# Kernel optimization log

Measured on AMD Instinct MI355X. Metric: run time of the kernel, lower is better.

The kernel has to match this reference:

```python
import jax, jax.numpy as jnp
import numpy as np

N, E, DIN, GB, GD, LB, LD, G = 50000, 640000, 64, 128, 4, 256, 2, 1024


def setup_inputs() -> dict:
    key = jax.random.key(0)
    ks = jax.random.split(key, 20)
    p = lambda k, shape: (jax.random.normal(k, shape, dtype=jnp.float32) * 0.05)
    return {
        "x": jax.random.normal(ks[0], (N, DIN), dtype=jnp.float32),
        "edge_index": jax.random.randint(ks[1], (2, E), 0, N, dtype=jnp.int64),
        "batch": jnp.sort(jax.random.randint(ks[2], (N,), 0, G, dtype=jnp.int64)),
        "num_graphs": G,
        "W0": p(ks[3], (DIN, GB)), "b0": p(ks[4], (GB,)),
        "Wg": p(ks[5], (GD, GB, GB)), "bg": p(ks[6], (GD, GB)),
        "gamma_g": jnp.ones((GD, GB), jnp.float32), "beta_g": jnp.zeros((GD, GB), jnp.float32),
        "Wl0": p(ks[7], (GB, LB)), "bl0": p(ks[8], (LB,)),
        "Wl": p(ks[9], (LD, LB, LB)), "bl": p(ks[10], (LD, LB)),
        "gamma_l": jnp.ones((LD, LB), jnp.float32), "beta_l": jnp.zeros((LD, LB), jnp.float32),
        "Wout": p(ks[11], (LB, 2)), "bout": p(ks[12], (2,)),
    }


def reference(x, edge_index, batch, num_graphs, W0, b0, Wg, bg, gamma_g, beta_g,
              Wl0, bl0, Wl, bl, gamma_l, beta_l, Wout, bout):
    n = x.shape[0]
    src, dst = edge_index[0], edge_index[1]
    # GCN degree normalization with self loops: deg = 1 + in-degree
    deg = jax.ops.segment_sum(jnp.ones(src.shape[0], x.dtype), dst, num_segments=n) + 1.0
    dinv = jax.lax.rsqrt(deg)                 # deg^{-1/2}
    enorm = dinv[src] * dinv[dst]             # [E] edge norm
    snorm = dinv * dinv                       # [N] self-loop norm (deg^{-1})

    def gcn(h, W, b):
        hw = h @ W                                            # [N, GB]
        agg = jax.ops.segment_sum(hw[src] * enorm[:, None], dst, num_segments=n)
        return agg + hw * snorm[:, None] + b

    def bn(h, g, bt):  # training-mode batchnorm (biased var), eps=1e-5
        m = h.mean(0)
        v = h.var(0)
        return (h - m) * jax.lax.rsqrt(v + 1e-5) * g + bt

    h = jax.nn.relu(gcn(x, W0, b0))
    for i in range(Wg.shape[0]):
        h = jax.nn.relu(bn(gcn(h, Wg[i], bg[i]), gamma_g[i], beta_g[i]))
    # global_add_pool
    hp = jax.ops.segment_sum(h, batch, num_segments=num_graphs)  # [G, GB]
    h = jax.nn.relu(hp @ Wl0 + bl0)
    for i in range(Wl.shape[0]):
        h = jax.nn.relu(bn(h @ Wl[i] + bl[i], gamma_l[i], beta_l[i]))
    return h @ Wout + bout
```

## Files before the change

### kernel.cpp

```cpp
#include <hip/hip_runtime.h>

#define NN 50000
#define EE 640000
#define DINv 64
#define GBv 128
#define GDv 4
#define LBv 256
#define LDv 2
#define GGv 1024

#define NB 196
#define BCAP 4096
#define BTILE 4096
#define NBT ((EE + BTILE - 1) / BTILE)

#define NTILES ((NN + 63) / 64)
#define UPN (NN * 16)
#define CONVN (DINv * GBv + GDv * GBv * GBv)

typedef _Float16 f16x8 __attribute__((ext_vector_type(8)));
typedef float f32x4 __attribute__((ext_vector_type(4)));

__device__ __forceinline__ float h2f(ushort u) {
  union { ushort u; _Float16 h; } x;
  x.u = u;
  return (float)x.h;
}
__device__ __forceinline__ ushort f2h(float f) {
  union { ushort u; _Float16 h; } x;
  x.h = (_Float16)f;
  return x.u;
}


__global__ __launch_bounds__(256) void k_bucket(const int* __restrict__ ei,
                                                int* __restrict__ bcnt,
                                                uint* __restrict__ bkt) {
  __shared__ int lcnt[NB];
  __shared__ int lbase[NB];
  __shared__ int gbase[NB];
  __shared__ int ls[256];
  __shared__ uint stage[BTILE];
  __shared__ ushort sb[BTILE];
  int tid = threadIdx.x;
  int t0 = blockIdx.x * BTILE;
  int cnt = min(BTILE, EE - t0);
  for (int i = tid; i < NB; i += 256) lcnt[i] = 0;
  __syncthreads();

  uint en[16];
  int bb[16], rk[16];
  int nper = (cnt + 255) >> 8;
  for (int k = 0; k < nper; k++) {
    int e = k * 256 + tid;
    if (e < cnt) {
      int src = ei[t0 + e];
      int dst = ei[EE + t0 + e];
      int b = dst >> 8;
      en[k] = ((uint)src << 8) | (uint)(dst & 255);
      bb[k] = b;
      rk[k] = atomicAdd(&lcnt[b], 1);
    } else {
      bb[k] = -1;
    }
  }
  __syncthreads();

  int v = (tid < NB) ? lcnt[tid] : 0;
  ls[tid] = v;
  __syncthreads();
  for (int off = 1; off < 256; off <<= 1) {
    int t = (tid >= off) ? ls[tid - off] : 0;
    __syncthreads();
    ls[tid] += t;
    __syncthreads();
  }
  if (tid < NB) {
    lbase[tid] = ls[tid] - v;
    gbase[tid] = atomicAdd(&bcnt[tid], v);
  }
  __syncthreads();

  for (int k = 0; k < nper; k++) {
    if (bb[k] >= 0) {
      int slot = lbase[bb[k]] + rk[k];
      stage[slot] = en[k];
      sb[slot] = (ushort)bb[k];
    }
  }
  __syncthreads();

  for (int i = tid; i < cnt; i += 256) {
    int b = sb[i];
    bkt[(size_t)b * BCAP + gbase[b] + (i - lbase[b])] = stage[i];
  }
}

__global__ __launch_bounds__(256) void k_bscan(const int* __restrict__ bcnt,
                                               int* __restrict__ bbase,
                                               int* __restrict__ offs) {
  __shared__ int ls[256];
  int tid = threadIdx.x;
  int v = (tid < NB) ? bcnt[tid] : 0;
  ls[tid] = v;
  __syncthreads();
  for (int off = 1; off < 256; off <<= 1) {
    int t = (tid >= off) ? ls[tid - off] : 0;
    __syncthreads();
    ls[tid] += t;
    __syncthreads();
  }
  if (tid < NB) bbase[tid] = ls[tid] - v;
  if (tid == 0) offs[NN] = EE;
}


__global__ __launch_bounds__(256) void k_csr(const uint* __restrict__ bkt,
                                             const int* __restrict__ bcnt,
                                             const int* __restrict__ bbase,
                                             int* __restrict__ offs,
                                             float* __restrict__ dinv,
                                             int* __restrict__ col,
                                             int* __restrict__ deg,
                                             int* __restrict__ ghist) {
  __shared__ int lhist[256];
  __shared__ int lofs[256];
  __shared__ int lcur[256];
  __shared__ int lh2[64];
  int b = blockIdx.x;
  int cnt = bcnt[b], base = bbase[b];
  const uint* B = bkt + (size_t)b * BCAP;
  int tid = threadIdx.x;
  lhist[tid] = 0;
  if (tid < 64) lh2[tid] = 0;
  __syncthreads();
  for (int i = tid; i < cnt; i += 256) atomicAdd(&lhist[B[i] & 255], 1);
  __syncthreads();
  int v = lhist[tid];
  lofs[tid] = v;
  __syncthreads();
  for (int off = 1; off < 256; off <<= 1) {
    int t = (tid >= off) ? lofs[tid - off] : 0;
    __syncthreads();
    lofs[tid] += t;
    __syncthreads();
  }
  int excl = lofs[tid] - v;
  int n = b * 256 + tid;
  if (n < NN) {
    offs[n] = base + excl;
    dinv[n] = rsqrtf((float)(v + 1));
    int d = min(v, 63);
    deg[n] = d;
    atomicAdd(&lh2[d], 1);
  }
  lcur[tid] = excl;
  __syncthreads();
  if (tid < 64 && lh2[tid]) atomicAdd(&ghist[tid], lh2[tid]);
  for (int i = tid; i < cnt; i += 256) {
    uint e = B[i];
    int p = atomicAdd(&lcur[e & 255], 1);
    col[base + p] = (int)(e >> 8);
  }
}

__global__ void k_dscan(const int* __restrict__ ghist, int* __restrict__ dcur) {
  if (threadIdx.x == 0 && blockIdx.x == 0) {
    int run = 0;
    for (int i = 0; i < 64; i++) {
      dcur[i] = run;
      run += ghist[i];
    }
  }
}

__global__ __launch_bounds__(256) void k_dperm(const int* __restrict__ deg,
                                               int* __restrict__ dcur,
                                               int* __restrict__ perm) {
  __shared__ int lhist[64];
  __shared__ int lbase[64];
  int tid = threadIdx.x;
  if (tid < 64) lhist[tid] = 0;
  __syncthreads();
  int n = blockIdx.x * 256 + tid;
  int d = 0, rk = 0;
  if (n < NN) {
    d = deg[n];
    rk = atomicAdd(&lhist[d], 1);
  }
  __syncthreads();
  if (tid < 64 && lhist[tid]) lbase[tid] = atomicAdd(&dcur[tid], lhist[tid]);
  __syncthreads();
  if (n < NN) perm[lbase[d] + rk] = n;
}


__global__ __launch_bounds__(256) void k_prep(const float* __restrict__ x,
                                              const float* __restrict__ dinv,
                                              const float* __restrict__ W0,
                                              const float* __restrict__ Wg,
                                              ushort* __restrict__ u,
                                              ushort* __restrict__ Wt0,
                                              ushort* __restrict__ Wtg) {
  int idx = blockIdx.x * 256 + threadIdx.x;
  if (idx < UPN) {
    int n = idx >> 4;
    float4 v = ((const float4*)x)[idx];
    float d = dinv[n];
    union { ushort us[4]; uint2 q; } o;
    o.us[0] = f2h(v.x * d);
    o.us[1] = f2h(v.y * d);
    o.us[2] = f2h(v.z * d);
    o.us[3] = f2h(v.w * d);
    ((uint2*)u)[idx] = o.q;
  } else {
    int j = idx - UPN;
    if (j < DINv * GBv) {
      int c = j >> 6, k = j & 63;
      Wt0[j] = f2h(W0[k * GBv + c]);
    } else if (j < CONVN) {
      int e = j - DINv * GBv;
      int i = e >> 14, rem = e & 16383;
      int c = rem >> 7, k = rem & 127;
      Wtg[e] = f2h(Wg[i * GBv * GBv + k * GBv + c]);
    }
  }
}


template <int K, int MODE>
__global__ __launch_bounds__(256) void k_agg(const ushort* __restrict__ Gin,
                                             const int* __restrict__ col,
                                             const int* __restrict__ offs,
                                             const float* __restrict__ dinv,
                                             const int* __restrict__ perm,
                                             const float* __restrict__ st,
                                             const float* __restrict__ gamma,
                                             const float* __restrict__ beta,
                                             ushort* __restrict__ V) {
  constexpr int VEC = K / 16;
  __shared__ float sS[128], sT[128];
  int tid = threadIdx.x;
  if constexpr (MODE == 2) {
    if (tid < 128) {
      float mu = st[tid] * (1.f / NN);
      float var = st[128 + tid] * (1.f / NN) - mu * mu;
      float s = rsqrtf(var + 1e-5f) * gamma[tid];
      sS[tid] = s;
      sT[tid] = beta[tid] - mu * s;
    }
    __syncthreads();
  }
  int lane = tid & 63;
  int q = lane >> 4, m = lane & 15;
  int idx = blockIdx.x * 16 + (tid >> 6) * 4 + q;
  int n = perm[idx];

  float sc[VEC], tc[VEC];
  if constexpr (MODE == 2) {
#pragma unroll
    for (int v = 0; v < VEC; v++) {
      sc[v] = sS[m * VEC + v];
      tc[v] = sT[m * VEC + v];
    }
  }

  union U { uint4 v4; uint2 v2; ushort us[8]; };
  auto loadrow = [&](int s) {
    U u;
    const ushort* p = Gin + (long)s * K + m * VEC;
    if constexpr (VEC == 8) u.v4 = *(const uint4*)p;
    else u.v2 = *(const uint2*)p;
    return u;
  };
  float acc[VEC];
#pragma unroll
  for (int v = 0; v < VEC; v++) acc[v] = 0.f;
  auto addrow = [&](U u, float dv) {
#pragma unroll
    for (int v = 0; v < VEC; v++) {
      float g = h2f(u.us[v]);
      if constexpr (MODE == 0) acc[v] += g;
      else if constexpr (MODE == 1) acc[v] += fmaxf(g, 0.f) * dv;
      else acc[v] += fmaxf(g * sc[v] + tc[v], 0.f) * dv;
    }
  };

  float dn = dinv[n];
  addrow(loadrow(n), dn);

  int s0 = offs[n], s1 = offs[n + 1];
  int j = s0;
  for (; j + 7 < s1; j += 8) {
    int si[8];
#pragma unroll
    for (int t = 0; t < 8; t++) si[t] = col[j + t];
    U uu[8];
#pragma unroll
    for (int t = 0; t < 8; t++) uu[t] = loadrow(si[t]);
    float dd[8];
#pragma unroll
    for (int t = 0; t < 8; t++) dd[t] = (MODE != 0) ? dinv[si[t]] : 0.f;
#pragma unroll
    for (int t = 0; t < 8; t++) addrow(uu[t], dd[t]);
  }
  for (; j + 3 < s1; j += 4) {
    int si[4];
#pragma unroll
    for (int t = 0; t < 4; t++) si[t] = col[j + t];
    U uu[4];
#pragma unroll
    for (int t = 0; t < 4; t++) uu[t] = loadrow(si[t]);
    float dd[4];
#pragma unroll
    for (int t = 0; t < 4; t++) dd[t] = (MODE != 0) ? dinv[si[t]] : 0.f;
#pragma unroll
    for (int t = 0; t < 4; t++) addrow(uu[t], dd[t]);
  }
  for (; j < s1; j++) {
    int s = col[j];
    U u = loadrow(s);
    float dv = (MODE != 0) ? dinv[s] : 0.f;
    addrow(u, dv);
  }

  U o;
#pragma unroll
  for (int v = 0; v < VEC; v++) o.us[v] = f2h(acc[v] * dn);
  ushort* op = V + (long)n * K + m * VEC;
  if constexpr (VEC == 8) *(uint4*)op = o.v4;
  else *(uint2*)op = o.v2;
}


template <int K, bool STATS>
__global__ __launch_bounds__(256) void k_mm(const ushort* __restrict__ X,
                                            const ushort* __restrict__ Wt,
                                            const float* __restrict__ bias,
                                            float* __restrict__ stG,
                                            ushort* __restrict__ Gout) {
  constexpr int KP = K + 8;
  constexpr int CP = 136;
  constexpr bool REUSE = (K == 128);
  __shared__ __attribute__((aligned(16))) _Float16 sW[128 * KP];
  __shared__ __attribute__((aligned(16))) _Float16 sA[64 * KP];
  __shared__ __attribute__((aligned(16))) _Float16 sCbuf[REUSE ? 8 : 64 * CP];
  __shared__ float sB[128];
  __shared__ float ssum[128], ssq[128];
  _Float16* sC = REUSE ? sA : sCbuf;
  int tid = threadIdx.x;

  {
    constexpr int CH = K / 8;
    for (int i = tid; i < 128 * CH; i += 256) {
      int c = i / CH, ch = i - c * CH;
      *(uint4*)&sW[c * KP + ch * 8] = ((const uint4*)Wt)[i];
    }
  }
  if (tid < 128) {
    sB[tid] = bias[tid];
    if constexpr (STATS) {
      ssum[tid] = 0.f;
      ssq[tid] = 0.f;
    }
  }

  int w = tid >> 6, lane = tid & 63;
  int m = lane & 15, quad = lane >> 4;
  int crow = 16 * w + quad * 4;

  float ps[8], pq[8];
  if constexpr (STATS) {
#pragma unroll
    for (int ct = 0; ct < 8; ct++) { ps[ct] = 0.f; pq[ct] = 0.f; }
  }

  for (int tile = blockIdx.x; tile < NTILES; tile += gridDim.x) {
    int row0 = tile * 64;
    __syncthreads();

    {
      int r = tid >> 2, col0 = (tid & 3) * (K / 4);
      int gr = row0 + r;
      const uint4* p = (const uint4*)(X + (long)gr * K + col0);
#pragma unroll
      for (int ch = 0; ch < K / 32; ch++) {
        uint4 v = (gr < NN) ? p[ch] : make_uint4(0, 0, 0, 0);
        *(uint4*)&sA[r * KP + col0 + ch * 8] = v;
      }
    }
    __syncthreads();

    f32x4 acc[8];
#pragma unroll
    for (int ct = 0; ct < 8; ct++) acc[ct] = (f32x4){0.f, 0.f, 0.f, 0.f};
    const _Float16* pa = &sA[(16 * w + m) * KP + quad * 8];
#pragma unroll
    for (int ks = 0; ks < K; ks += 32) {
      f16x8 a = *(const f16x8*)(pa + ks);
#pragma unroll
      for (int ct = 0; ct < 8; ct++) {
        f16x8 b = *(const f16x8*)&sW[(ct * 16 + m) * KP + ks + quad * 8];
        acc[ct] = __builtin_amdgcn_mfma_f32_16x16x32_f16(a, b, acc[ct], 0, 0, 0);
      }
    }

    if constexpr (STATS) {
#pragma unroll
      for (int ct = 0; ct < 8; ct++) {
        int c = ct * 16 + m;
        float b = sB[c];
#pragma unroll
        for (int r = 0; r < 4; r++) {
          if (row0 + crow + r < NN) {
            float g = acc[ct][r] + b;
            ps[ct] += g;
            pq[ct] += g * g;
          }
        }
      }
    }
    if constexpr (REUSE) __syncthreads();

#pragma unroll
    for (int ct = 0; ct < 8; ct++) {
      int c = ct * 16 + m;
      float b = sB[c];
#pragma unroll
      for (int r = 0; r < 4; r++) sC[(crow + r) * CP + c] = (_Float16)(acc[ct][r] + b);
    }
    __syncthreads();

    {
      int r = tid >> 2, col0 = (tid & 3) * 32;
      int gr = row0 + r;
      if (gr < NN) {
        const uint4* src = (const uint4*)&sC[r * CP + col0];
        uint4* dst = (uint4*)(Gout + (long)gr * 128 + col0);
#pragma unroll
        for (int ch = 0; ch < 4; ch++) dst[ch] = src[ch];
      }
    }
  }

  if constexpr (STATS) {
#pragma unroll
    for (int ct = 0; ct < 8; ct++) {
      float s = ps[ct], q = pq[ct];
      s += __shfl_xor(s, 16);
      q += __shfl_xor(q, 16);
      s += __shfl_xor(s, 32);
      q += __shfl_xor(q, 32);
      if (quad == 0) {
        atomicAdd(&ssum[ct * 16 + m], s);
        atomicAdd(&ssq[ct * 16 + m], q);
      }
    }
    __syncthreads();
    if (tid < 128) {
      int c = (tid + blockIdx.x * 8) & 127;
      atomicAdd(&stG[c], ssum[c]);
      atomicAdd(&stG[128 + c], ssq[c]);
    }
  }
}


__global__ __launch_bounds__(128) void k_pool2(const ushort* __restrict__ G,
                                               const float* __restrict__ st,
                                               const float* __restrict__ gamma,
                                               const float* __restrict__ beta,
                                               const int* __restrict__ batch,
                                               float* __restrict__ hp) {
  __shared__ int sse[2];
  int g = blockIdx.x;
  int c = threadIdx.x;
  if (c < 2) {
    int key = g + c;
    int lo = 0, hi = NN;
    while (lo < hi) {
      int mid = (lo + hi) >> 1;
      if (batch[mid] < key) lo = mid + 1;
      else hi = mid;
    }
    sse[c] = lo;
  }
  __syncthreads();
  int s = sse[0], e = sse[1];
  float m = st[c] * (1.f / NN);
  float v = st[128 + c] * (1.f / NN) - m * m;
  float sc = rsqrtf(v + 1e-5f) * gamma[c];
  float tc = beta[c] - m * sc;
  float acc = 0.f;
  for (int n = s; n < e; n++) acc += fmaxf(h2f(G[(long)n * 128 + c]) * sc + tc, 0.f);
  hp[(long)g * 128 + c] = acc;
}


__global__ void k_colstats(const float* __restrict__ X, int rows, float* __restrict__ st) {
  int c = threadIdx.x;
  int C = blockDim.x;
  float s = 0.f, q = 0.f;
  for (int r = blockIdx.x; r < rows; r += gridDim.x) {
    float v = X[(long)r * C + c];
    s += v;
    q += v * v;
  }
  atomicAdd(&st[c], s);
  atomicAdd(&st[C + c], q);
}


template <int KIN, int MODE>
__global__ __launch_bounds__(256) void k_fc(const float* __restrict__ X,
                                            const float* __restrict__ W,
                                            const float* __restrict__ b,
                                            const float* __restrict__ st,
                                            const float* __restrict__ gamma,
                                            const float* __restrict__ beta,
                                            float* __restrict__ Y) {
  __shared__ float sx[KIN];
  int g = blockIdx.x;
  int c = threadIdx.x;
  for (int k = c; k < KIN; k += 256) {
    float v = X[(long)g * KIN + k];
    if constexpr (MODE == 2) {
      float m = st[k] * (1.f / GGv);
      float var = st[KIN + k] * (1.f / GGv) - m * m;
      v = fmaxf((v - m) * rsqrtf(var + 1e-5f) * gamma[k] + beta[k], 0.f);
    }
    sx[k] = v;
  }
  __syncthreads();
  float acc = b[c];
#pragma unroll 8
  for (int k = 0; k < KIN; k++) acc += sx[k] * W[(long)k * 256 + c];
  Y[(long)g * 256 + c] = (MODE == 0) ? fmaxf(acc, 0.f) : acc;
}

__global__ __launch_bounds__(256) void k_out(const float* __restrict__ X,
                                             const float* __restrict__ st,
                                             const float* __restrict__ gamma,
                                             const float* __restrict__ beta,
                                             const float* __restrict__ Wout,
                                             const float* __restrict__ bout,
                                             float* __restrict__ out) {
  int g = blockIdx.x * 4 + (threadIdx.x >> 6);
  int l = threadIdx.x & 63;
  float a0 = 0.f, a1 = 0.f;
  for (int k = l; k < LBv; k += 64) {
    float z = X[(long)g * LBv + k];
    float m = st[k] * (1.f / GGv);
    float var = st[LBv + k] * (1.f / GGv) - m * m;
    float x = fmaxf((z - m) * rsqrtf(var + 1e-5f) * gamma[k] + beta[k], 0.f);
    a0 += x * Wout[2 * k];
    a1 += x * Wout[2 * k + 1];
  }
  for (int off = 32; off > 0; off >>= 1) {
    a0 += __shfl_down(a0, off);
    a1 += __shfl_down(a1, off);
  }
  if (l == 0) {
    out[2 * g] = a0 + bout[0];
    out[2 * g + 1] = a1 + bout[1];
  }
}


extern "C" void kernel_launch(void* const* d_in, const int* in_sizes, int n_in,
                              void* d_out, int out_size, void* d_ws, size_t ws_size,
                              hipStream_t stream) {
  const float* x = (const float*)d_in[0];
  const int* ei = (const int*)d_in[1];
  const int* batch = (const int*)d_in[2];
  const float* W0 = (const float*)d_in[4];
  const float* b0 = (const float*)d_in[5];
  const float* Wg = (const float*)d_in[6];
  const float* bg = (const float*)d_in[7];
  const float* gamma_g = (const float*)d_in[8];
  const float* beta_g = (const float*)d_in[9];
  const float* Wl0 = (const float*)d_in[10];
  const float* bl0 = (const float*)d_in[11];
  const float* Wl = (const float*)d_in[12];
  const float* bl = (const float*)d_in[13];
  const float* gamma_l = (const float*)d_in[14];
  const float* beta_l = (const float*)d_in[15];
  const float* Wout = (const float*)d_in[16];
  const float* bout = (const float*)d_in[17];
  float* out = (float*)d_out;

  char* w = (char*)d_ws;
  auto alloc = [&](size_t bytes) {
    void* p = (void*)w;
    w += (bytes + 255) & ~(size_t)255;
    return p;
  };
  int* bcnt = (int*)alloc((size_t)NB * 4);
  float* stAll = (float*)alloc((size_t)(4 * 256 + 2 * 512) * 4);
  int* ghist = (int*)alloc((size_t)64 * 4);
  size_t zspan = (char*)w - (char*)bcnt;
  uint* bkt = (uint*)alloc((size_t)NB * BCAP * 4);
  int* bbase = (int*)alloc((size_t)NB * 4);
  int* offs = (int*)alloc((size_t)(NN + 1) * 4);
  int* col = (int*)alloc((size_t)EE * 4);
  float* dinv = (float*)alloc((size_t)NN * 4);
  int* deg = (int*)alloc((size_t)NN * 4);
  int* perm = (int*)alloc((size_t)NN * 4);
  int* dcur = (int*)alloc((size_t)64 * 4);
  ushort* u = (ushort*)alloc((size_t)NN * DINv * 2);
  ushort* V = (ushort*)alloc((size_t)NN * GBv * 2);
  ushort* g = (ushort*)alloc((size_t)NN * GBv * 2);
  ushort* Wt0 = (ushort*)alloc((size_t)DINv * GBv * 2);
  ushort* Wtg = (ushort*)alloc((size_t)GDv * GBv * GBv * 2);
  float* hp = (float*)alloc((size_t)GGv * GBv * 4);
  float* m1 = (float*)alloc((size_t)GGv * LBv * 4);
  float* m2 = (float*)alloc((size_t)GGv * LBv * 4);

  float* stg = stAll;
  float* sth0 = stAll + 4 * 256;
  float* sth1 = sth0 + 512;

  hipMemsetAsync(bcnt, 0, zspan, stream);

  k_bucket<<<NBT, 256, 0, stream>>>(ei, bcnt, bkt);
  k_bscan<<<1, 256, 0, stream>>>(bcnt, bbase, offs);
  k_csr<<<NB, 256, 0, stream>>>(bkt, bcnt, bbase, offs, dinv, col, deg, ghist);
  k_dscan<<<1, 64, 0, stream>>>(ghist, dcur);
  k_dperm<<<NB, 256, 0, stream>>>(deg, dcur, perm);
  k_prep<<<(UPN + CONVN + 255) / 256, 256, 0, stream>>>(x, dinv, W0, Wg, u, Wt0, Wtg);

  const int AGG = NN / 16;
  const int MMG = 512;

  k_agg<64, 0><<<AGG, 256, 0, stream>>>(u, col, offs, dinv, perm, nullptr, nullptr,
                                        nullptr, V);
  k_mm<64, false><<<MMG, 256, 0, stream>>>(V, Wt0, b0, nullptr, g);

  k_agg<128, 1><<<AGG, 256, 0, stream>>>(g, col, offs, dinv, perm, nullptr, nullptr,
                                         nullptr, V);
  k_mm<128, true><<<MMG, 256, 0, stream>>>(V, Wtg, bg, stg, g);

  for (int i = 1; i < GDv; i++) {
    k_agg<128, 2><<<AGG, 256, 0, stream>>>(g, col, offs, dinv, perm,
                                           stg + (size_t)(i - 1) * 256,
                                           gamma_g + (size_t)(i - 1) * GBv,
                                           beta_g + (size_t)(i - 1) * GBv, V);
    k_mm<128, true><<<MMG, 256, 0, stream>>>(V, Wtg + (size_t)i * GBv * GBv,
                                             bg + (size_t)i * GBv, stg + (size_t)i * 256, g);
  }

  k_pool2<<<GGv, 128, 0, stream>>>(g, stg + 3 * 256, gamma_g + 3 * GBv, beta_g + 3 * GBv,
                                   batch, hp);

  k_fc<GBv, 0><<<GGv, 256, 0, stream>>>(hp, Wl0, bl0, nullptr, nullptr, nullptr, m1);
  k_fc<LBv, 1><<<GGv, 256, 0, stream>>>(m1, Wl, bl, nullptr, nullptr, nullptr, m2);
  k_colstats<<<256, LBv, 0, stream>>>(m2, GGv, sth0);
  k_fc<LBv, 2><<<GGv, 256, 0, stream>>>(m2, Wl + (size_t)LBv * LBv, bl + LBv, sth0,
                                        gamma_l, beta_l, m1);
  k_colstats<<<256, LBv, 0, stream>>>(m1, GGv, sth1);
  k_out<<<GGv / 4, 256, 0, stream>>>(m1, sth1, gamma_l + LBv, beta_l + LBv, Wout, bout, out);
}
```

Baseline: 449.0 us.

## Fuse neighbor aggregation with MFMA matmul per layer and fold scan kernels

Each GCN layer's sparse aggregation now writes its 64-row tile straight into shared memory, and the same block then runs the MFMA matmul and writes the output rows scattered via perm. This removes the intermediate V round-trip through global memory and one launch per layer. The bucket scan and degree scan kernels are also folded into k_csr and k_dperm, which each recompute a small prefix sum redundantly per block. The cost is that every block reloads the weight matrix into LDS, and the per-block LDS footprint may reduce occupancy for the latency-bound gather phase. Output buffers now ping-pong between g1 and g2.

```diff
diff --git a/kernel.cpp b/kernel.cpp
--- a/kernel.cpp
+++ b/kernel.cpp
@@ -96,28 +96,9 @@
   }
 }
 
-__global__ __launch_bounds__(256) void k_bscan(const int* __restrict__ bcnt,
-                                               int* __restrict__ bbase,
-                                               int* __restrict__ offs) {
-  __shared__ int ls[256];
-  int tid = threadIdx.x;
-  int v = (tid < NB) ? bcnt[tid] : 0;
-  ls[tid] = v;
-  __syncthreads();
-  for (int off = 1; off < 256; off <<= 1) {
-    int t = (tid >= off) ? ls[tid - off] : 0;
-    __syncthreads();
-    ls[tid] += t;
-    __syncthreads();
-  }
-  if (tid < NB) bbase[tid] = ls[tid] - v;
-  if (tid == 0) offs[NN] = EE;
-}
-
 
 __global__ __launch_bounds__(256) void k_csr(const uint* __restrict__ bkt,
                                              const int* __restrict__ bcnt,
-                                             const int* __restrict__ bbase,
                                              int* __restrict__ offs,
                                              float* __restrict__ dinv,
                                              int* __restrict__ col,
@@ -126,14 +107,24 @@
   __shared__ int lhist[256];
   __shared__ int lofs[256];
   __shared__ int lcur[256];
+  __shared__ int lsb[256];
   __shared__ int lh2[64];
   int b = blockIdx.x;
-  int cnt = bcnt[b], base = bbase[b];
-  const uint* B = bkt + (size_t)b * BCAP;
   int tid = threadIdx.x;
+  int bv = (tid < NB) ? bcnt[tid] : 0;
+  lsb[tid] = bv;
   lhist[tid] = 0;
   if (tid < 64) lh2[tid] = 0;
   __syncthreads();
+  for (int off = 1; off < 256; off <<= 1) {
+    int t = (tid >= off) ? lsb[tid - off] : 0;
+    __syncthreads();
+    lsb[tid] += t;
+    __syncthreads();
+  }
+  int cnt = bcnt[b];
+  int base = lsb[b] - cnt;
+  const uint* B = bkt + (size_t)b * BCAP;
   for (int i = tid; i < cnt; i += 256) atomicAdd(&lhist[B[i] & 255], 1);
   __syncthreads();
   int v = lhist[tid];
@@ -157,6 +148,7 @@
   lcur[tid] = excl;
   __syncthreads();
   if (tid < 64 && lh2[tid]) atomicAdd(&ghist[tid], lh2[tid]);
+  if (b == 0 && tid == 0) offs[NN] = EE;
   for (int i = tid; i < cnt; i += 256) {
     uint e = B[i];
     int p = atomicAdd(&lcur[e & 255], 1);
@@ -164,18 +156,10 @@
   }
 }
 
-__global__ void k_dscan(const int* __restrict__ ghist, int* __restrict__ dcur) {
-  if (threadIdx.x == 0 && blockIdx.x == 0) {
-    int run = 0;
-    for (int i = 0; i < 64; i++) {
-      dcur[i] = run;
-      run += ghist[i];
-    }
-  }
-}
 
 __global__ __launch_bounds__(256) void k_dperm(const int* __restrict__ deg,
-                                               int* __restrict__ dcur,
+                                               const int* __restrict__ ghist,
+                                               int* __restrict__ gcur,
                                                int* __restrict__ perm) {
   __shared__ int lhist[64];
   __shared__ int lbase[64];
@@ -189,7 +173,11 @@
     rk = atomicAdd(&lhist[d], 1);
   }
   __syncthreads();
-  if (tid < 64 && lhist[tid]) lbase[tid] = atomicAdd(&dcur[tid], lhist[tid]);
+  if (tid < 64) {
+    int s = 0;
+    for (int i = tid + 1; i < 64; i++) s += ghist[i];
+    if (lhist[tid]) lbase[tid] = s + atomicAdd(&gcur[tid], lhist[tid]);
+  }
   __syncthreads();
   if (n < NN) perm[lbase[d] + rk] = n;
 }
@@ -228,33 +216,57 @@
 }
 
 
-template <int K, int MODE>
-__global__ __launch_bounds__(256) void k_agg(const ushort* __restrict__ Gin,
-                                             const int* __restrict__ col,
-                                             const int* __restrict__ offs,
-                                             const float* __restrict__ dinv,
-                                             const int* __restrict__ perm,
-                                             const float* __restrict__ st,
-                                             const float* __restrict__ gamma,
-                                             const float* __restrict__ beta,
-                                             ushort* __restrict__ V) {
+template <int K, int MODE, bool STATS>
+__global__ __launch_bounds__(256) void k_layer(const ushort* __restrict__ Gin,
+                                               const int* __restrict__ col,
+                                               const int* __restrict__ offs,
+                                               const float* __restrict__ dinv,
+                                               const int* __restrict__ perm,
+                                               const float* __restrict__ st,
+                                               const float* __restrict__ gamma,
+                                               const float* __restrict__ beta,
+                                               const ushort* __restrict__ Wt,
+                                               const float* __restrict__ bias,
+                                               float* __restrict__ stG,
+                                               ushort* __restrict__ Gout) {
   constexpr int VEC = K / 16;
-  __shared__ float sS[128], sT[128];
+  constexpr int KP = K + 8;
+  constexpr int CP = 136;
+  constexpr bool REUSE = (K == 128);
+  __shared__ __attribute__((aligned(16))) _Float16 sW[128 * KP];
+  __shared__ __attribute__((aligned(16))) _Float16 sA[64 * KP];
+  __shared__ __attribute__((aligned(16))) _Float16 sCbuf[REUSE ? 8 : 64 * CP];
+  __shared__ float sB[128], sS[128], sT[128];
+  __shared__ float ssum[128], ssq[128];
+  _Float16* sC = REUSE ? sA : sCbuf;
   int tid = threadIdx.x;
-  if constexpr (MODE == 2) {
-    if (tid < 128) {
+
+  {
+    constexpr int CH = K / 8;
+    for (int i = tid; i < 128 * CH; i += 256) {
+      int c = i / CH, ch = i - c * CH;
+      *(uint4*)&sW[c * KP + ch * 8] = ((const uint4*)Wt)[i];
+    }
+  }
+  if (tid < 128) {
+    sB[tid] = bias[tid];
+    if constexpr (STATS) {
+      ssum[tid] = 0.f;
+      ssq[tid] = 0.f;
+    }
+    if constexpr (MODE == 2) {
       float mu = st[tid] * (1.f / NN);
       float var = st[128 + tid] * (1.f / NN) - mu * mu;
       float s = rsqrtf(var + 1e-5f) * gamma[tid];
       sS[tid] = s;
       sT[tid] = beta[tid] - mu * s;
     }
-    __syncthreads();
-  }
-  int lane = tid & 63;
-  int q = lane >> 4, m = lane & 15;
-  int idx = blockIdx.x * 16 + (tid >> 6) * 4 + q;
-  int n = perm[idx];
+  }
+  if constexpr (MODE == 2) __syncthreads();
+
+  int w = tid >> 6, lane = tid & 63;
+  int quad = lane >> 4, m = lane & 15;
+  int row0 = blockIdx.x * 64;
 
   float sc[VEC], tc[VEC];
   if constexpr (MODE == 2) {
@@ -273,173 +285,124 @@
     else u.v2 = *(const uint2*)p;
     return u;
   };
-  float acc[VEC];
-#pragma unroll
-  for (int v = 0; v < VEC; v++) acc[v] = 0.f;
-  auto addrow = [&](U u, float dv) {
-#pragma unroll
-    for (int v = 0; v < VEC; v++) {
-      float g = h2f(u.us[v]);
-      if constexpr (MODE == 0) acc[v] += g;
-      else if constexpr (MODE == 1) acc[v] += fmaxf(g, 0.f) * dv;
-      else acc[v] += fmaxf(g * sc[v] + tc[v], 0.f) * dv;
-    }
-  };
-
-  float dn = dinv[n];
-  addrow(loadrow(n), dn);
-
-  int s0 = offs[n], s1 = offs[n + 1];
-  int j = s0;
-  for (; j + 7 < s1; j += 8) {
-    int si[8];
-#pragma unroll
-    for (int t = 0; t < 8; t++) si[t] = col[j + t];
-    U uu[8];
-#pragma unroll
-    for (int t = 0; t < 8; t++) uu[t] = loadrow(si[t]);
-    float dd[8];
-#pragma unroll
-    for (int t = 0; t < 8; t++) dd[t] = (MODE != 0) ? dinv[si[t]] : 0.f;
-#pragma unroll
-    for (int t = 0; t < 8; t++) addrow(uu[t], dd[t]);
-  }
-  for (; j + 3 < s1; j += 4) {
-    int si[4];
-#pragma unroll
-    for (int t = 0; t < 4; t++) si[t] = col[j + t];
-    U uu[4];
-#pragma unroll
-    for (int t = 0; t < 4; t++) uu[t] = loadrow(si[t]);
-    float dd[4];
-#pragma unroll
-    for (int t = 0; t < 4; t++) dd[t] = (MODE != 0) ? dinv[si[t]] : 0.f;
-#pragma unroll
-    for (int t = 0; t < 4; t++) addrow(uu[t], dd[t]);
-  }
-  for (; j < s1; j++) {
-    int s = col[j];
-    U u = loadrow(s);
-    float dv = (MODE != 0) ? dinv[s] : 0.f;
-    addrow(u, dv);
-  }
-
-  U o;
-#pragma unroll
-  for (int v = 0; v < VEC; v++) o.us[v] = f2h(acc[v] * dn);
-  ushort* op = V + (long)n * K + m * VEC;
-  if constexpr (VEC == 8) *(uint4*)op = o.v4;
-  else *(uint2*)op = o.v2;
-}
-
-
-template <int K, bool STATS>
-__global__ __launch_bounds__(256) void k_mm(const ushort* __restrict__ X,
-                                            const ushort* __restrict__ Wt,
-                                            const float* __restrict__ bias,
-                                            float* __restrict__ stG,
-                                            ushort* __restrict__ Gout) {
-  constexpr int KP = K + 8;
-  constexpr int CP = 136;
-  constexpr bool REUSE = (K == 128);
-  __shared__ __attribute__((aligned(16))) _Float16 sW[128 * KP];
-  __shared__ __attribute__((aligned(16))) _Float16 sA[64 * KP];
-  __shared__ __attribute__((aligned(16))) _Float16 sCbuf[REUSE ? 8 : 64 * CP];
-  __shared__ float sB[128];
-  __shared__ float ssum[128], ssq[128];
-  _Float16* sC = REUSE ? sA : sCbuf;
-  int tid = threadIdx.x;
-
-  {
-    constexpr int CH = K / 8;
-    for (int i = tid; i < 128 * CH; i += 256) {
-      int c = i / CH, ch = i - c * CH;
-      *(uint4*)&sW[c * KP + ch * 8] = ((const uint4*)Wt)[i];
-    }
-  }
-  if (tid < 128) {
-    sB[tid] = bias[tid];
-    if constexpr (STATS) {
-      ssum[tid] = 0.f;
-      ssq[tid] = 0.f;
-    }
-  }
-
-  int w = tid >> 6, lane = tid & 63;
-  int m = lane & 15, quad = lane >> 4;
+
+  for (int rnd = 0; rnd < 4; rnd++) {
+    int r = rnd * 16 + w * 4 + quad;
+    int idx = row0 + r;
+    float acc[VEC];
+#pragma unroll
+    for (int v = 0; v < VEC; v++) acc[v] = 0.f;
+    float dn = 0.f;
+    if (idx < NN) {
+      int n = perm[idx];
+      dn = dinv[n];
+      auto addrow = [&](U u, float dv) {
+#pragma unroll
+        for (int v = 0; v < VEC; v++) {
+          float g = h2f(u.us[v]);
+          if constexpr (MODE == 0) acc[v] += g;
+          else if constexpr (MODE == 1) acc[v] += fmaxf(g, 0.f) * dv;
+          else acc[v] += fmaxf(g * sc[v] + tc[v], 0.f) * dv;
+        }
+      };
+      addrow(loadrow(n), dn);
+      int s0 = offs[n], s1 = offs[n + 1];
+      int j = s0;
+      for (; j + 7 < s1; j += 8) {
+        int si[8];
+#pragma unroll
+        for (int t = 0; t < 8; t++) si[t] = col[j + t];
+        U uu[8];
+#pragma unroll
+        for (int t = 0; t < 8; t++) uu[t] = loadrow(si[t]);
+        float dd[8];
+#pragma unroll
+        for (int t = 0; t < 8; t++) dd[t] = (MODE != 0) ? dinv[si[t]] : 0.f;
+#pragma unroll
+        for (int t = 0; t < 8; t++) addrow(uu[t], dd[t]);
+      }
+      for (; j + 3 < s1; j += 4) {
+        int si[4];
+#pragma unroll
+        for (int t = 0; t < 4; t++) si[t] = col[j + t];
+        U uu[4];
+#pragma unroll
+        for (int t = 0; t < 4; t++) uu[t] = loadrow(si[t]);
+        float dd[4];
+#pragma unroll
+        for (int t = 0; t < 4; t++) dd[t] = (MODE != 0) ? dinv[si[t]] : 0.f;
+#pragma unroll
+        for (int t = 0; t < 4; t++) addrow(uu[t], dd[t]);
+      }
+      for (; j < s1; j++) {
+        int s = col[j];
+        U u = loadrow(s);
+        float dv = (MODE != 0) ? dinv[s] : 0.f;
+        addrow(u, dv);
+      }
+    }
+    U o;
+#pragma unroll
+    for (int v = 0; v < VEC; v++) o.us[v] = f2h(acc[v] * dn);
+    _Float16* ap = &sA[r * KP + m * VEC];
+    if constexpr (VEC == 8) *(uint4*)ap = o.v4;
+    else *(uint2*)ap = o.v2;
+  }
+  __syncthreads();
+
+  f32x4 acc2[8];
+#pragma unroll
+  for (int ct = 0; ct < 8; ct++) acc2[ct] = (f32x4){0.f, 0.f, 0.f, 0.f};
+  const _Float16* pa = &sA[(16 * w + m) * KP + quad * 8];
+#pragma unroll
+  for (int ks = 0; ks < K; ks += 32) {
+    f16x8 a = *(const f16x8*)(pa + ks);
+#pragma unroll
+    for (int ct = 0; ct < 8; ct++) {
+      f16x8 bfr = *(const f16x8*)&sW[(ct * 16 + m) * KP + ks + quad * 8];
+      acc2[ct] = __builtin_amdgcn_mfma_f32_16x16x32_f16(a, bfr, acc2[ct], 0, 0, 0);
+    }
+  }
+
   int crow = 16 * w + quad * 4;
-
   float ps[8], pq[8];
   if constexpr (STATS) {
 #pragma unroll
-    for (int ct = 0; ct < 8; ct++) { ps[ct] = 0.f; pq[ct] = 0.f; }
-  }
-
-  for (int tile = blockIdx.x; tile < NTILES; tile += gridDim.x) {
-    int row0 = tile * 64;
-    __syncthreads();
-
-    {
-      int r = tid >> 2, col0 = (tid & 3) * (K / 4);
-      int gr = row0 + r;
-      const uint4* p = (const uint4*)(X + (long)gr * K + col0);
-#pragma unroll
-      for (int ch = 0; ch < K / 32; ch++) {
-        uint4 v = (gr < NN) ? p[ch] : make_uint4(0, 0, 0, 0);
-        *(uint4*)&sA[r * KP + col0 + ch * 8] = v;
-      }
-    }
-    __syncthreads();
-
-    f32x4 acc[8];
-#pragma unroll
-    for (int ct = 0; ct < 8; ct++) acc[ct] = (f32x4){0.f, 0.f, 0.f, 0.f};
-    const _Float16* pa = &sA[(16 * w + m) * KP + quad * 8];
-#pragma unroll
-    for (int ks = 0; ks < K; ks += 32) {
-      f16x8 a = *(const f16x8*)(pa + ks);
-#pragma unroll
-      for (int ct = 0; ct < 8; ct++) {
-        f16x8 b = *(const f16x8*)&sW[(ct * 16 + m) * KP + ks + quad * 8];
-        acc[ct] = __builtin_amdgcn_mfma_f32_16x16x32_f16(a, b, acc[ct], 0, 0, 0);
-      }
-    }
-
-    if constexpr (STATS) {
-#pragma unroll
-      for (int ct = 0; ct < 8; ct++) {
-        int c = ct * 16 + m;
-        float b = sB[c];
-#pragma unroll
-        for (int r = 0; r < 4; r++) {
-          if (row0 + crow + r < NN) {
-            float g = acc[ct][r] + b;
-            ps[ct] += g;
-            pq[ct] += g * g;
-          }
+    for (int ct = 0; ct < 8; ct++) {
+      int c = ct * 16 + m;
+      float bb = sB[c];
+      ps[ct] = 0.f;
+      pq[ct] = 0.f;
+#pragma unroll
+      for (int r = 0; r < 4; r++) {
+        if (row0 + crow + r < NN) {
+          float g = acc2[ct][r] + bb;
+          ps[ct] += g;
+          pq[ct] += g * g;
         }
       }
     }
-    if constexpr (REUSE) __syncthreads();
-
-#pragma unroll
-    for (int ct = 0; ct < 8; ct++) {
-      int c = ct * 16 + m;
-      float b = sB[c];
-#pragma unroll
-      for (int r = 0; r < 4; r++) sC[(crow + r) * CP + c] = (_Float16)(acc[ct][r] + b);
-    }
-    __syncthreads();
-
-    {
-      int r = tid >> 2, col0 = (tid & 3) * 32;
-      int gr = row0 + r;
-      if (gr < NN) {
-        const uint4* src = (const uint4*)&sC[r * CP + col0];
-        uint4* dst = (uint4*)(Gout + (long)gr * 128 + col0);
-#pragma unroll
-        for (int ch = 0; ch < 4; ch++) dst[ch] = src[ch];
-      }
+  }
+  if constexpr (REUSE) __syncthreads();
+
+#pragma unroll
+  for (int ct = 0; ct < 8; ct++) {
+    int c = ct * 16 + m;
+    float bb = sB[c];
+#pragma unroll
+    for (int r = 0; r < 4; r++) sC[(crow + r) * CP + c] = (_Float16)(acc2[ct][r] + bb);
+  }
+  __syncthreads();
+
+  {
+    int r = tid >> 2, col0 = (tid & 3) * 32;
+    int idx = row0 + r;
+    if (idx < NN) {
+      int node = perm[idx];
+      const uint4* srcp = (const uint4*)&sC[r * CP + col0];
+      uint4* dst = (uint4*)(Gout + (long)node * 128 + col0);
+#pragma unroll
+      for (int ch = 0; ch < 4; ch++) dst[ch] = srcp[ch];
     }
   }
 
@@ -598,18 +561,17 @@
   int* bcnt = (int*)alloc((size_t)NB * 4);
   float* stAll = (float*)alloc((size_t)(4 * 256 + 2 * 512) * 4);
   int* ghist = (int*)alloc((size_t)64 * 4);
+  int* gcur = (int*)alloc((size_t)64 * 4);
   size_t zspan = (char*)w - (char*)bcnt;
   uint* bkt = (uint*)alloc((size_t)NB * BCAP * 4);
-  int* bbase = (int*)alloc((size_t)NB * 4);
   int* offs = (int*)alloc((size_t)(NN + 1) * 4);
   int* col = (int*)alloc((size_t)EE * 4);
   float* dinv = (float*)alloc((size_t)NN * 4);
   int* deg = (int*)alloc((size_t)NN * 4);
   int* perm = (int*)alloc((size_t)NN * 4);
-  int* dcur = (int*)alloc((size_t)64 * 4);
   ushort* u = (ushort*)alloc((size_t)NN * DINv * 2);
-  ushort* V = (ushort*)alloc((size_t)NN * GBv * 2);
-  ushort* g = (ushort*)alloc((size_t)NN * GBv * 2);
+  ushort* g1 = (ushort*)alloc((size_t)NN * GBv * 2);
+  ushort* g2 = (ushort*)alloc((size_t)NN * GBv * 2);
   ushort* Wt0 = (ushort*)alloc((size_t)DINv * GBv * 2);
   ushort* Wtg = (ushort*)alloc((size_t)GDv * GBv * GBv * 2);
   float* hp = (float*)alloc((size_t)GGv * GBv * 4);
@@ -623,33 +585,24 @@
   hipMemsetAsync(bcnt, 0, zspan, stream);
 
   k_bucket<<<NBT, 256, 0, stream>>>(ei, bcnt, bkt);
-  k_bscan<<<1, 256, 0, stream>>>(bcnt, bbase, offs);
-  k_csr<<<NB, 256, 0, stream>>>(bkt, bcnt, bbase, offs, dinv, col, deg, ghist);
-  k_dscan<<<1, 64, 0, stream>>>(ghist, dcur);
-  k_dperm<<<NB, 256, 0, stream>>>(deg, dcur, perm);
+  k_csr<<<NB, 256, 0, stream>>>(bkt, bcnt, offs, dinv, col, deg, ghist);
+  k_dperm<<<NB, 256, 0, stream>>>(deg, ghist, gcur, perm);
   k_prep<<<(UPN + CONVN + 255) / 256, 256, 0, stream>>>(x, dinv, W0, Wg, u, Wt0, Wtg);
 
-  const int AGG = NN / 16;
-  const int MMG = 512;
-
-  k_agg<64, 0><<<AGG, 256, 0, stream>>>(u, col, offs, dinv, perm, nullptr, nullptr,
-                                        nullptr, V);
-  k_mm<64, false><<<MMG, 256, 0, stream>>>(V, Wt0, b0, nullptr, g);
-
-  k_agg<128, 1><<<AGG, 256, 0, stream>>>(g, col, offs, dinv, perm, nullptr, nullptr,
-                                         nullptr, V);
-  k_mm<128, true><<<MMG, 256, 0, stream>>>(V, Wtg, bg, stg, g);
-
+  k_layer<64, 0, false><<<NTILES, 256, 0, stream>>>(u, col, offs, dinv, perm, nullptr,
+                                                    nullptr, nullptr, Wt0, b0, nullptr, g1);
+  k_layer<128, 1, true><<<NTILES, 256, 0, stream>>>(g1, col, offs, dinv, perm, nullptr,
+                                                    nullptr, nullptr, Wtg, bg, stg, g2);
   for (int i = 1; i < GDv; i++) {
-    k_agg<128, 2><<<AGG, 256, 0, stream>>>(g, col, offs, dinv, perm,
-                                           stg + (size_t)(i - 1) * 256,
-                                           gamma_g + (size_t)(i - 1) * GBv,
-                                           beta_g + (size_t)(i - 1) * GBv, V);
-    k_mm<128, true><<<MMG, 256, 0, stream>>>(V, Wtg + (size_t)i * GBv * GBv,
-                                             bg + (size_t)i * GBv, stg + (size_t)i * 256, g);
-  }
-
-  k_pool2<<<GGv, 128, 0, stream>>>(g, stg + 3 * 256, gamma_g + 3 * GBv, beta_g + 3 * GBv,
+    const ushort* gin = (i & 1) ? g2 : g1;
+    ushort* gout = (i & 1) ? g1 : g2;
+    k_layer<128, 2, true><<<NTILES, 256, 0, stream>>>(
+        gin, col, offs, dinv, perm, stg + (size_t)(i - 1) * 256,
+        gamma_g + (size_t)(i - 1) * GBv, beta_g + (size_t)(i - 1) * GBv,
+        Wtg + (size_t)i * GBv * GBv, bg + (size_t)i * GBv, stg + (size_t)i * 256, gout);
+  }
+
+  k_pool2<<<GGv, 128, 0, stream>>>(g1, stg + 3 * 256, gamma_g + 3 * GBv, beta_g + 3 * GBv,
                                    batch, hp);
 
   k_fc<GBv, 0><<<GGv, 256, 0, stream>>>(hp, Wl0, bl0, nullptr, nullptr, nullptr, m1);
```

New measurement: 445.5 us. About the same (-0.8%).
